# Optimization experiments

Hardware: AMD Instinct MI355X
Metric: run time of the kernel (lower is better)

Reference implementation:

```python
import jax, jax.numpy as jnp
import numpy as np

N = 60000      # total nodes
D = 300        # feature dim
R = 5          # num relations == num bases
E = 1_000_000  # edges
S = 25000      # last_idx_senses
G = 50000      # last_idx_globals
BATCH = 32


def setup_inputs() -> dict:
    key = jax.random.key(0)
    ks = jax.random.split(key, 12)
    x = jax.random.normal(ks[0], (N, D), dtype=jnp.float32)
    edge_index = jax.random.randint(ks[1], (2, E), 0, N, dtype=jnp.int32)
    edge_type = jax.random.randint(ks[2], (E,), 0, R, dtype=jnp.int32)
    current_node_index = jax.random.randint(ks[3], (BATCH,), 0, N, dtype=jnp.int32)
    scale = 1.0 / np.sqrt(D)
    # RGCNConv basis decomposition params (num_bases == num_relations)
    basis = jax.random.normal(ks[4], (R, D, D), dtype=jnp.float32) * scale
    comp = jax.random.normal(ks[5], (R, R), dtype=jnp.float32) * scale
    root = jax.random.normal(ks[6], (D, D), dtype=jnp.float32) * scale
    bias = jnp.zeros((D,), dtype=jnp.float32)
    # heads
    w_global = jax.random.normal(ks[7], (G - S, D), dtype=jnp.float32) * scale
    b_global = jnp.zeros((G - S,), dtype=jnp.float32)
    w_sense = jax.random.normal(ks[8], (S, D), dtype=jnp.float32) * scale
    b_sense = jnp.zeros((S,), dtype=jnp.float32)
    return {
        "x": x, "edge_index": edge_index, "edge_type": edge_type,
        "current_node_index": current_node_index,
        "basis": basis, "comp": comp, "root": root, "bias": bias,
        "w_global": w_global, "b_global": b_global,
        "w_sense": w_sense, "b_sense": b_sense,
    }


def reference(x, edge_index, edge_type, current_node_index,
              basis, comp, root, bias,
              w_global, b_global, w_sense, b_sense):
    src, dst = edge_index[0], edge_index[1]
    # Combined segment id over (dst node, relation): mean-aggregate source
    # features per (node, relation), then apply the per-relation transform
    # (mean(x_j) @ W_r == mean(x_j @ W_r); matches PyG RGCNConv aggr='mean').
    seg = dst * R + edge_type                      # [E]
    msg_sum = jax.ops.segment_sum(x[src], seg, num_segments=N * R)  # [N*R, D]
    cnt = jax.ops.segment_sum(jnp.ones((E,), jnp.float32), seg, num_segments=N * R)
    mean = msg_sum.reshape(N, R, D) / jnp.maximum(cnt.reshape(N, R, 1), 1.0)
    # basis decomposition: W_r = sum_b comp[r,b] * basis[b]
    W = jnp.einsum('rb,bij->rij', comp, basis)     # [R, D, D]
    agg = jnp.einsum('nrd,rde->ne', mean, W)       # [N, D]
    h = jax.nn.relu(agg + x @ root + bias)         # [N, D]
    hc = h[current_node_index]                     # [B, D]
    logits_global = hc @ w_global.T + b_global     # [B, G-S]
    logits_sense = hc @ w_sense.T + b_sense        # [B, S]
    return (jax.nn.log_softmax(logits_global, axis=-1),
            jax.nn.log_softmax(logits_sense, axis=-1))
```

## Files before the change

kernel.cpp:

```cpp
#include <hip/hip_runtime.h>
#include <hip/hip_bf16.h>
#include <math.h>

#define D 300
#define R 5
#define NE 1000000
#define B 32
#define NG 25000
#define NS 25000
#define NROWS 50000
#define NT16 3125

typedef __bf16 bf16x8 __attribute__((ext_vector_type(8)));
typedef float f32x4 __attribute__((ext_vector_type(4)));


__device__ __forceinline__ void online_upd(float& m, float& s, float v) {
    if (v > m) { s = s * __expf(m - v) + 1.0f; m = v; }
    else       { s += __expf(v - m); }
}
__device__ __forceinline__ void online_merge(float& m, float& s, float om, float os) {
    float M = fmaxf(m, om);
    s = s * __expf(m - M) + os * __expf(om - M);
    m = M;
}

__global__ void zero_ws(float4* __restrict__ p) {
    int i = blockIdx.x * 256 + threadIdx.x;
    if (i < 14441) p[i] = float4{0.f, 0.f, 0.f, 0.f};
}

__global__ __launch_bounds__(256) void scan_accum(
        const int* __restrict__ ei, const int* __restrict__ et,
        const int* __restrict__ cur, const float* __restrict__ x,
        float* __restrict__ wsum, float* __restrict__ wcnt) {
    __shared__ unsigned int tbl[32];
    __shared__ int curl[B];
    __shared__ int lcnt;
    __shared__ int2 loc[64];
    int tid = threadIdx.x;
    if (tid < 32) tbl[tid] = 0u;
    if (tid == 0) lcnt = 0;
    __syncthreads();
    if (tid < B) { int c = cur[tid]; curl[tid] = c; atomicOr(&tbl[(c >> 5) & 31], 1u << (c & 31)); }
    __syncthreads();
    long base = ((long)blockIdx.x * 256 + tid) * 4;
    if (base < NE) {
        int ds4[4];
        if (base + 4 <= NE) {
            int4 d4 = *(const int4*)(ei + NE + base);
            ds4[0] = d4.x; ds4[1] = d4.y; ds4[2] = d4.z; ds4[3] = d4.w;
        } else {
            for (int k = 0; k < 4; ++k) ds4[k] = (base + k < NE) ? ei[NE + base + k] : -1;
        }
        #pragma unroll
        for (int k = 0; k < 4; ++k) {
            int dst = ds4[k];
            if (dst < 0) continue;
            if (!(tbl[(dst >> 5) & 31] & (1u << (dst & 31)))) continue;
            int e = (int)base + k;
            int r = -1, src = 0;
            for (int b = 0; b < B; ++b) {
                if (dst == curl[b]) {
                    if (r < 0) { r = et[e]; src = ei[e]; }
                    atomicAdd(&wcnt[b * R + r], 1.0f);
                    int p = atomicAdd(&lcnt, 1);
                    if (p < 64) loc[p] = int2{src, b * R + r};
                }
            }
        }
    }
    __syncthreads();
    int n = lcnt; if (n > 64) n = 64;
    for (int m = 0; m < n; ++m) {
        int2 pr = loc[m];
        const float* xs = x + (long)pr.x * D;
        float* sm = wsum + (long)pr.y * D;
        for (int t = tid; t < D; t += 256) atomicAdd(&sm[t], xs[t]);
    }
}

__global__ __launch_bounds__(320) void rgcn_hc(
        const float* __restrict__ x, const int* __restrict__ cur,
        const float* __restrict__ comp, const float* __restrict__ root,
        const float* __restrict__ basis, const float* __restrict__ bias,
        const float* __restrict__ wsum, const float* __restrict__ wcnt,
        float* __restrict__ hcf, int* __restrict__ done, __bf16* __restrict__ hcb) {
    int kc = blockIdx.x, t = threadIdx.x;
    __shared__ float uL[800];
    __shared__ float inv[B * R];
    __shared__ float cmp[R * R];
    __shared__ int lastFlag;
    if (t < B * R) inv[t] = 1.0f / fmaxf(wcnt[t], 1.0f);
    if (t >= 160 && t < 160 + R * R) cmp[t - 160] = comp[t - 160];
    __syncthreads();
    int d0 = kc * 25;
    if (d0 < 300) {
        for (int i = t; i < 800; i += 320) {
            int b = i / 25, dd = i - b * 25;
            uL[i] = x[(long)cur[b] * D + d0 + dd];
        }
    } else {
        int g0 = d0 - 300;
        int bb = g0 / 300, t0 = g0 - bb * 300;
        for (int i = t; i < 800; i += 320) {
            int b = i / 25, dd = i - b * 25;
            float a = 0.f;
            #pragma unroll
            for (int r = 0; r < R; ++r)
                a = fmaf(cmp[r * R + bb] * inv[b * R + r], wsum[(long)(b * R + r) * D + t0 + dd], a);
            uL[i] = a;
        }
    }
    __syncthreads();
    if (t < D) {
        const float* Mb = (d0 < 300) ? (root + (long)d0 * D) : (basis + (long)(d0 - 300) * D);
        float acc[B] = {};
        #pragma unroll 5
        for (int i = 0; i < 25; ++i) {
            float m = Mb[(long)i * D + t];
            #pragma unroll
            for (int b = 0; b < B; ++b) acc[b] = fmaf(uL[b * 25 + i], m, acc[b]);
        }
        for (int b = 0; b < B; ++b) atomicAdd(&hcf[b * D + t], acc[b]);
    }
    __syncthreads();
    if (t == 0) {
        __threadfence();
        int p = atomicAdd(done, 1);
        lastFlag = (p == 71);
    }
    __syncthreads();
    if (!lastFlag) return;
    __threadfence();
    for (int i = t; i < 32 * 320; i += 320) {
        int b = i / 320, kk = i - b * 320;
        float a = 0.f;
        if (kk < D) a = fmaxf(atomicAdd(&hcf[b * D + kk], 0.0f) + bias[kk], 0.f);
        hcb[i] = (__bf16)a;
    }
}

__global__ __launch_bounds__(64) void head_gemm16(
    const __bf16* __restrict__ hcb, const float* __restrict__ wg, const float* __restrict__ bg,
    const float* __restrict__ wsn, const float* __restrict__ bsn,
    float* __restrict__ out, float2* __restrict__ pm2) {
    int l = threadIdx.x;
    int jt = blockIdx.x;
    int j0 = jt * 16;
    int ln = l & 15, og = l >> 4;

    bf16x8 bfrag0[10], bfrag1[10];
    const __bf16* hrow0 = hcb + ln * 320 + og * 8;
    const __bf16* hrow1 = hcb + (16 + ln) * 320 + og * 8;
    #pragma unroll
    for (int s = 0; s < 10; ++s) {
        bfrag0[s] = *(const bf16x8*)(hrow0 + 32 * s);
        bfrag1[s] = *(const bf16x8*)(hrow1 + 32 * s);
    }

    int row = j0 + ln;
    const float* wrow = ((row < NG) ? (wg + (long)row * D) : (wsn + (long)(row - NG) * D)) + og * 8;

    f32x4 acc0 = {}, acc1 = {};
    #pragma unroll
    for (int s = 0; s < 9; ++s) {
        float4 w0 = *(const float4*)(wrow + 32 * s);
        float4 w1 = *(const float4*)(wrow + 32 * s + 4);
        bf16x8 a;
        a[0]=(__bf16)w0.x; a[1]=(__bf16)w0.y; a[2]=(__bf16)w0.z; a[3]=(__bf16)w0.w;
        a[4]=(__bf16)w1.x; a[5]=(__bf16)w1.y; a[6]=(__bf16)w1.z; a[7]=(__bf16)w1.w;
        acc0 = __builtin_amdgcn_mfma_f32_16x16x32_bf16(a, bfrag0[s], acc0, 0, 0, 0);
        acc1 = __builtin_amdgcn_mfma_f32_16x16x32_bf16(a, bfrag1[s], acc1, 0, 0, 0);
    }
    {
        float4 w0 = float4{0.f,0.f,0.f,0.f}, w1 = float4{0.f,0.f,0.f,0.f};
        if (og == 0) { w0 = *(const float4*)(wrow + 288); w1 = *(const float4*)(wrow + 292); }
        else if (og == 1) { w0 = *(const float4*)(wrow + 288); }
        bf16x8 a;
        a[0]=(__bf16)w0.x; a[1]=(__bf16)w0.y; a[2]=(__bf16)w0.z; a[3]=(__bf16)w0.w;
        a[4]=(__bf16)w1.x; a[5]=(__bf16)w1.y; a[6]=(__bf16)w1.z; a[7]=(__bf16)w1.w;
        acc0 = __builtin_amdgcn_mfma_f32_16x16x32_bf16(a, bfrag0[9], acc0, 0, 0, 0);
        acc1 = __builtin_amdgcn_mfma_f32_16x16x32_bf16(a, bfrag1[9], acc1, 0, 0, 0);
    }

    int b0 = ln, b1 = 16 + ln;
    float m0 = -3.0e38f, s0 = 0.f, m1 = -3.0e38f, s1 = 0.f;
    float m2 = -3.0e38f, s2 = 0.f, m3 = -3.0e38f, s3 = 0.f;
    #pragma unroll
    for (int r = 0; r < 4; ++r) {
        int j = j0 + og * 4 + r;
        float bv = (j < NG) ? bg[j] : bsn[j - NG];
        float v0 = acc0[r] + bv;
        float v1 = acc1[r] + bv;
        float* op0 = (j < NG) ? (out + (long)b0 * NG + j)
                              : (out + (long)B * NG + (long)b0 * NS + (j - NG));
        float* op1 = (j < NG) ? (out + (long)b1 * NG + j)
                              : (out + (long)B * NG + (long)b1 * NS + (j - NG));
        *op0 = v0;
        *op1 = v1;
        if (j < NG) { online_upd(m0, s0, v0); online_upd(m2, s2, v1); }
        else        { online_upd(m1, s1, v0); online_upd(m3, s3, v1); }
    }
    #pragma unroll
    for (int o = 16; o <= 32; o <<= 1) {
        float t;
        t = __shfl_xor(m0, o); { float ts = __shfl_xor(s0, o); online_merge(m0, s0, t, ts); }
        t = __shfl_xor(m1, o); { float ts = __shfl_xor(s1, o); online_merge(m1, s1, t, ts); }
        t = __shfl_xor(m2, o); { float ts = __shfl_xor(s2, o); online_merge(m2, s2, t, ts); }
        t = __shfl_xor(m3, o); { float ts = __shfl_xor(s3, o); online_merge(m3, s3, t, ts); }
    }
    if (og == 0) {
        pm2[(long)b0 * NT16 + jt]       = float2{m0, s0};
        pm2[(long)(B + b0) * NT16 + jt] = float2{m1, s1};
        pm2[(long)b1 * NT16 + jt]       = float2{m2, s2};
        pm2[(long)(B + b1) * NT16 + jt] = float2{m3, s3};
    }
}

__global__ __launch_bounds__(256) void lse_red(const float2* __restrict__ pm2,
                                               float* __restrict__ lse) {
    int rw = blockIdx.x, tid = threadIdx.x;
    const float2* pr = pm2 + (long)rw * NT16;
    float m = -3.0e38f, s = 0.f;
    for (int i = tid; i < NT16; i += 256) { float2 e = pr[i]; online_merge(m, s, e.x, e.y); }
    #pragma unroll
    for (int o = 32; o; o >>= 1) {
        float om = __shfl_xor(m, o), os = __shfl_xor(s, o);
        online_merge(m, s, om, os);
    }
    __shared__ float sm[4], ss[4];
    if ((tid & 63) == 0) { sm[tid >> 6] = m; ss[tid >> 6] = s; }
    __syncthreads();
    if (tid == 0) {
        float M = sm[0], S = ss[0];
        for (int w = 1; w < 4; ++w) online_merge(M, S, sm[w], ss[w]);
        lse[rw] = M + __logf(S);
    }
}

__global__ __launch_bounds__(256) void sub_lse(float* __restrict__ out,
                                               const float* __restrict__ lse) {
    int rw = blockIdx.x / 25, c = blockIdx.x % 25;
    float l = lse[rw];
    float4* o4 = (float4*)out + (long)rw * 6250 + c * 250;
    int tid = threadIdx.x;
    if (tid < 250) { float4 v = o4[tid]; v.x -= l; v.y -= l; v.z -= l; v.w -= l; o4[tid] = v; }
}

extern "C" void kernel_launch(void* const* d_in, const int* in_sizes, int n_in,
                              void* d_out, int out_size, void* d_ws, size_t ws_size,
                              hipStream_t stream) {
    const float* x     = (const float*)d_in[0];
    const int*   ei    = (const int*)d_in[1];
    const int*   et    = (const int*)d_in[2];
    const int*   cur   = (const int*)d_in[3];
    const float* basis = (const float*)d_in[4];
    const float* comp  = (const float*)d_in[5];
    const float* root  = (const float*)d_in[6];
    const float* bias  = (const float*)d_in[7];
    const float* wg    = (const float*)d_in[8];
    const float* bgl   = (const float*)d_in[9];
    const float* wsn   = (const float*)d_in[10];
    const float* bsn   = (const float*)d_in[11];
    float* out  = (float*)d_out;
    float* wsf  = (float*)d_ws;
    float*  wsum = wsf;
    float*  wcnt = wsf + 48000;
    float*  hcf  = wsf + 48160;
    int*    done = (int*)(wsf + 57760);
    __bf16* hcb  = (__bf16*)(wsf + 57764);
    float2* pm2  = (float2*)(wsf + 62884);
    float*  lse  = wsf + 462884;

    zero_ws<<<57, 256, 0, stream>>>((float4*)d_ws);
    scan_accum<<<977, 256, 0, stream>>>(ei, et, cur, x, wsum, wcnt);
    rgcn_hc<<<72, 320, 0, stream>>>(x, cur, comp, root, basis, bias, wsum, wcnt, hcf, done, hcb);
    head_gemm16<<<NT16, 64, 0, stream>>>(hcb, wg, bgl, wsn, bsn, out, pm2);
    lse_red<<<64, 256, 0, stream>>>(pm2, lse);
    sub_lse<<<1600, 256, 0, stream>>>(out, lse);
}
```

Measured before the change: 80.29 us.

## Restructure pipeline: drop zero kernel, match-list scan, fuse finalize and LSE stages

The global zeroing kernel is removed; the edge scan now only records matching (src, slot) pairs per block into a compact list and zeroes hcf itself. Each rgcn_hc basis block gathers that list and accumulates neighbour sums and counts in shared memory, so the global atomics and the last-block finalize with its threadfence are gone. The ReLU/bias/bf16 conversion of hc moves into head_gemm, which now runs four waves per block and stages hc in padded LDS. The LSE reduction is merged with the subtraction. Together this cuts the launch count from six to four. The trade-off is that every basis block redundantly scans the match list and re-gathers x rows, and the per-block cap of 16 matches (1024 in total) could drop edges on heavier inputs.

```diff
diff --git a/kernel.cpp b/kernel.cpp
--- a/kernel.cpp
+++ b/kernel.cpp
@@ -10,6 +10,9 @@
 #define NS 25000
 #define NROWS 50000
 #define NT16 3125
+#define NSB 977
+#define MCAP 16
+#define HST 324
 
 typedef __bf16 bf16x8 __attribute__((ext_vector_type(8)));
 typedef float f32x4 __attribute__((ext_vector_type(4)));
@@ -25,20 +28,17 @@
     m = M;
 }
 
-__global__ void zero_ws(float4* __restrict__ p) {
-    int i = blockIdx.x * 256 + threadIdx.x;
-    if (i < 14441) p[i] = float4{0.f, 0.f, 0.f, 0.f};
-}
-
-__global__ __launch_bounds__(256) void scan_accum(
+__global__ __launch_bounds__(256) void scan_match(
         const int* __restrict__ ei, const int* __restrict__ et,
-        const int* __restrict__ cur, const float* __restrict__ x,
-        float* __restrict__ wsum, float* __restrict__ wcnt) {
+        const int* __restrict__ cur,
+        int2* __restrict__ mlist, int* __restrict__ mcntb, float* __restrict__ hcf) {
     __shared__ unsigned int tbl[32];
     __shared__ int curl[B];
     __shared__ int lcnt;
-    __shared__ int2 loc[64];
+    __shared__ int2 loc[MCAP];
     int tid = threadIdx.x;
+    int gidx = blockIdx.x * 256 + tid;
+    if (gidx < 9600) hcf[gidx] = 0.f;
     if (tid < 32) tbl[tid] = 0u;
     if (tid == 0) lcnt = 0;
     __syncthreads();
@@ -63,58 +63,81 @@
             for (int b = 0; b < B; ++b) {
                 if (dst == curl[b]) {
                     if (r < 0) { r = et[e]; src = ei[e]; }
-                    atomicAdd(&wcnt[b * R + r], 1.0f);
                     int p = atomicAdd(&lcnt, 1);
-                    if (p < 64) loc[p] = int2{src, b * R + r};
+                    if (p < MCAP) loc[p] = int2{src, b * R + r};
                 }
             }
         }
     }
     __syncthreads();
-    int n = lcnt; if (n > 64) n = 64;
-    for (int m = 0; m < n; ++m) {
-        int2 pr = loc[m];
-        const float* xs = x + (long)pr.x * D;
-        float* sm = wsum + (long)pr.y * D;
-        for (int t = tid; t < D; t += 256) atomicAdd(&sm[t], xs[t]);
-    }
+    int n = lcnt < MCAP ? lcnt : MCAP;
+    if (tid == 0) mcntb[blockIdx.x] = n;
+    if (tid < n) mlist[blockIdx.x * MCAP + tid] = loc[tid];
 }
 
 __global__ __launch_bounds__(320) void rgcn_hc(
         const float* __restrict__ x, const int* __restrict__ cur,
         const float* __restrict__ comp, const float* __restrict__ root,
-        const float* __restrict__ basis, const float* __restrict__ bias,
-        const float* __restrict__ wsum, const float* __restrict__ wcnt,
-        float* __restrict__ hcf, int* __restrict__ done, __bf16* __restrict__ hcb) {
+        const float* __restrict__ basis,
+        const int2* __restrict__ mlist, const int* __restrict__ mcntb,
+        float* __restrict__ hcf) {
     int kc = blockIdx.x, t = threadIdx.x;
     __shared__ float uL[800];
-    __shared__ float inv[B * R];
+    __shared__ int2 ml[1024];
+    __shared__ int mn;
+    __shared__ float wsumL[160 * 25];
+    __shared__ float cntL[160];
+    __shared__ float invL[160];
     __shared__ float cmp[R * R];
-    __shared__ int lastFlag;
-    if (t < B * R) inv[t] = 1.0f / fmaxf(wcnt[t], 1.0f);
-    if (t >= 160 && t < 160 + R * R) cmp[t - 160] = comp[t - 160];
-    __syncthreads();
     int d0 = kc * 25;
-    if (d0 < 300) {
+
+    if (kc < 12) {
         for (int i = t; i < 800; i += 320) {
             int b = i / 25, dd = i - b * 25;
             uL[i] = x[(long)cur[b] * D + d0 + dd];
         }
+        __syncthreads();
     } else {
-        int g0 = d0 - 300;
-        int bb = g0 / 300, t0 = g0 - bb * 300;
+        if (t == 0) mn = 0;
+        if (t < R * R) cmp[t] = comp[t];
+        for (int i = t; i < 160; i += 320) cntL[i] = 0.f;
+        for (int i = t; i < 160 * 25; i += 320) wsumL[i] = 0.f;
+        __syncthreads();
+        for (int i = t; i < NSB; i += 320) {
+            int c = mcntb[i];
+            for (int k = 0; k < c; ++k) {
+                int p = atomicAdd(&mn, 1);
+                if (p < 1024) ml[p] = mlist[i * MCAP + k];
+            }
+        }
+        __syncthreads();
+        int n = mn < 1024 ? mn : 1024;
+        for (int m = t; m < n; m += 320) atomicAdd(&cntL[ml[m].y], 1.0f);
+        __syncthreads();
+        for (int i = t; i < 160; i += 320) invL[i] = 1.0f / fmaxf(cntL[i], 1.0f);
+        int g2 = kc - 12;
+        int bb = g2 / 12, t0 = (g2 - bb * 12) * 25;
+        if (t < 300) {
+            int g = t / 25, col = t - g * 25;
+            for (int m = g; m < n; m += 12) {
+                int2 pr = ml[m];
+                atomicAdd(&wsumL[pr.y * 25 + col], x[(long)pr.x * D + t0 + col]);
+            }
+        }
+        __syncthreads();
         for (int i = t; i < 800; i += 320) {
             int b = i / 25, dd = i - b * 25;
             float a = 0.f;
             #pragma unroll
             for (int r = 0; r < R; ++r)
-                a = fmaf(cmp[r * R + bb] * inv[b * R + r], wsum[(long)(b * R + r) * D + t0 + dd], a);
+                a = fmaf(cmp[r * R + bb] * invL[b * R + r], wsumL[(b * R + r) * 25 + dd], a);
             uL[i] = a;
         }
-    }
-    __syncthreads();
+        __syncthreads();
+    }
+
     if (t < D) {
-        const float* Mb = (d0 < 300) ? (root + (long)d0 * D) : (basis + (long)(d0 - 300) * D);
+        const float* Mb = (kc < 12) ? (root + (long)d0 * D) : (basis + (long)(d0 - 300) * D);
         float acc[B] = {};
         #pragma unroll 5
         for (int i = 0; i < 25; ++i) {
@@ -124,35 +147,31 @@
         }
         for (int b = 0; b < B; ++b) atomicAdd(&hcf[b * D + t], acc[b]);
     }
-    __syncthreads();
-    if (t == 0) {
-        __threadfence();
-        int p = atomicAdd(done, 1);
-        lastFlag = (p == 71);
-    }
-    __syncthreads();
-    if (!lastFlag) return;
-    __threadfence();
-    for (int i = t; i < 32 * 320; i += 320) {
-        int b = i / 320, kk = i - b * 320;
-        float a = 0.f;
-        if (kk < D) a = fmaxf(atomicAdd(&hcf[b * D + kk], 0.0f) + bias[kk], 0.f);
-        hcb[i] = (__bf16)a;
-    }
-}
-
-__global__ __launch_bounds__(64) void head_gemm16(
-    const __bf16* __restrict__ hcb, const float* __restrict__ wg, const float* __restrict__ bg,
+}
+
+__global__ __launch_bounds__(256) void head_gemm(
+    const float* __restrict__ hcf, const float* __restrict__ bias,
+    const float* __restrict__ wg, const float* __restrict__ bg,
     const float* __restrict__ wsn, const float* __restrict__ bsn,
     float* __restrict__ out, float2* __restrict__ pm2) {
-    int l = threadIdx.x;
-    int jt = blockIdx.x;
+    __shared__ __bf16 hcbL[32 * HST];
+    int tid = threadIdx.x;
+    for (int i = tid; i < 32 * HST; i += 256) {
+        int b = i / HST, kk = i - b * HST;
+        float v = 0.f;
+        if (kk < D) v = fmaxf(hcf[b * D + kk] + bias[kk], 0.f);
+        hcbL[i] = (__bf16)v;
+    }
+    __syncthreads();
+
+    int wid = tid >> 6, l = tid & 63, ln = l & 15, og = l >> 4;
+    int jt = blockIdx.x * 4 + wid;
+    if (jt >= NT16) return;
     int j0 = jt * 16;
-    int ln = l & 15, og = l >> 4;
 
     bf16x8 bfrag0[10], bfrag1[10];
-    const __bf16* hrow0 = hcb + ln * 320 + og * 8;
-    const __bf16* hrow1 = hcb + (16 + ln) * 320 + og * 8;
+    const __bf16* hrow0 = hcbL + ln * HST + og * 8;
+    const __bf16* hrow1 = hcbL + (16 + ln) * HST + og * 8;
     #pragma unroll
     for (int s = 0; s < 10; ++s) {
         bfrag0[s] = *(const bf16x8*)(hrow0 + 32 * s);
@@ -204,11 +223,11 @@
     }
     #pragma unroll
     for (int o = 16; o <= 32; o <<= 1) {
-        float t;
-        t = __shfl_xor(m0, o); { float ts = __shfl_xor(s0, o); online_merge(m0, s0, t, ts); }
-        t = __shfl_xor(m1, o); { float ts = __shfl_xor(s1, o); online_merge(m1, s1, t, ts); }
-        t = __shfl_xor(m2, o); { float ts = __shfl_xor(s2, o); online_merge(m2, s2, t, ts); }
-        t = __shfl_xor(m3, o); { float ts = __shfl_xor(s3, o); online_merge(m3, s3, t, ts); }
+        float tm, ts;
+        tm = __shfl_xor(m0, o); ts = __shfl_xor(s0, o); online_merge(m0, s0, tm, ts);
+        tm = __shfl_xor(m1, o); ts = __shfl_xor(s1, o); online_merge(m1, s1, tm, ts);
+        tm = __shfl_xor(m2, o); ts = __shfl_xor(s2, o); online_merge(m2, s2, tm, ts);
+        tm = __shfl_xor(m3, o); ts = __shfl_xor(s3, o); online_merge(m3, s3, tm, ts);
     }
     if (og == 0) {
         pm2[(long)b0 * NT16 + jt]       = float2{m0, s0};
@@ -218,9 +237,10 @@
     }
 }
 
-__global__ __launch_bounds__(256) void lse_red(const float2* __restrict__ pm2,
-                                               float* __restrict__ lse) {
-    int rw = blockIdx.x, tid = threadIdx.x;
+__global__ __launch_bounds__(256) void lse_sub(float* __restrict__ out,
+                                               const float2* __restrict__ pm2) {
+    int rw = blockIdx.x / 25, c = blockIdx.x % 25;
+    int tid = threadIdx.x;
     const float2* pr = pm2 + (long)rw * NT16;
     float m = -3.0e38f, s = 0.f;
     for (int i = tid; i < NT16; i += 256) { float2 e = pr[i]; online_merge(m, s, e.x, e.y); }
@@ -230,21 +250,17 @@
         online_merge(m, s, om, os);
     }
     __shared__ float sm[4], ss[4];
+    __shared__ float lseS;
     if ((tid & 63) == 0) { sm[tid >> 6] = m; ss[tid >> 6] = s; }
     __syncthreads();
     if (tid == 0) {
         float M = sm[0], S = ss[0];
         for (int w = 1; w < 4; ++w) online_merge(M, S, sm[w], ss[w]);
-        lse[rw] = M + __logf(S);
-    }
-}
-
-__global__ __launch_bounds__(256) void sub_lse(float* __restrict__ out,
-                                               const float* __restrict__ lse) {
-    int rw = blockIdx.x / 25, c = blockIdx.x % 25;
-    float l = lse[rw];
+        lseS = M + __logf(S);
+    }
+    __syncthreads();
+    float l = lseS;
     float4* o4 = (float4*)out + (long)rw * 6250 + c * 250;
-    int tid = threadIdx.x;
     if (tid < 250) { float4 v = o4[tid]; v.x -= l; v.y -= l; v.z -= l; v.w -= l; o4[tid] = v; }
 }
 
@@ -265,18 +281,13 @@
     const float* bsn   = (const float*)d_in[11];
     float* out  = (float*)d_out;
     float* wsf  = (float*)d_ws;
-    float*  wsum = wsf;
-    float*  wcnt = wsf + 48000;
-    float*  hcf  = wsf + 48160;
-    int*    done = (int*)(wsf + 57760);
-    __bf16* hcb  = (__bf16*)(wsf + 57764);
-    float2* pm2  = (float2*)(wsf + 62884);
-    float*  lse  = wsf + 462884;
-
-    zero_ws<<<57, 256, 0, stream>>>((float4*)d_ws);
-    scan_accum<<<977, 256, 0, stream>>>(ei, et, cur, x, wsum, wcnt);
-    rgcn_hc<<<72, 320, 0, stream>>>(x, cur, comp, root, basis, bias, wsum, wcnt, hcf, done, hcb);
-    head_gemm16<<<NT16, 64, 0, stream>>>(hcb, wg, bgl, wsn, bsn, out, pm2);
-    lse_red<<<64, 256, 0, stream>>>(pm2, lse);
-    sub_lse<<<1600, 256, 0, stream>>>(out, lse);
-}
+    float*  hcf   = wsf;
+    float2* pm2   = (float2*)(wsf + 9600);
+    int*    mcntb = (int*)(wsf + 409600);
+    int2*   mlist = (int2*)(wsf + 410578);
+
+    scan_match<<<NSB, 256, 0, stream>>>(ei, et, cur, mlist, mcntb, hcf);
+    rgcn_hc<<<72, 320, 0, stream>>>(x, cur, comp, root, basis, mlist, mcntb, hcf);
+    head_gemm<<<(NT16 + 3) / 4, 256, 0, stream>>>(hcf, bias, wg, bgl, wsn, bsn, out, pm2);
+    lse_sub<<<1600, 256, 0, stream>>>(out, pm2);
+}
```

Measured after the change: 91.75 us. +14.3%, slower.

## Fuse bias/ReLU into head GEMM via LDS, merge LSE reduce with subtract

Applied to the files above, without the earlier changes.

Removes the last-block completion counter in rgcn_hc. Bias, ReLU and the bf16 conversion of hc now happen inside the head GEMM, which stages hc in padded LDS and runs four waves per block, each issuing all of its weight-row loads up front behind a sched_barrier. The separate LSE reduction kernel is merged into the subtract kernel, so each of the 1600 blocks recomputes its row's LSE from the partials. This cuts one launch and the serialized tail, at the cost of redundant LSE reductions and per-block hc staging.

```diff
diff --git a/kernel.cpp b/kernel.cpp
--- a/kernel.cpp
+++ b/kernel.cpp
@@ -10,6 +10,7 @@
 #define NS 25000
 #define NROWS 50000
 #define NT16 3125
+#define HST 324
 
 typedef __bf16 bf16x8 __attribute__((ext_vector_type(8)));
 typedef float f32x4 __attribute__((ext_vector_type(4)));
@@ -27,7 +28,7 @@
 
 __global__ void zero_ws(float4* __restrict__ p) {
     int i = blockIdx.x * 256 + threadIdx.x;
-    if (i < 14441) p[i] = float4{0.f, 0.f, 0.f, 0.f};
+    if (i < 14440) p[i] = float4{0.f, 0.f, 0.f, 0.f};
 }
 
 __global__ __launch_bounds__(256) void scan_accum(
@@ -83,14 +84,12 @@
 __global__ __launch_bounds__(320) void rgcn_hc(
         const float* __restrict__ x, const int* __restrict__ cur,
         const float* __restrict__ comp, const float* __restrict__ root,
-        const float* __restrict__ basis, const float* __restrict__ bias,
-        const float* __restrict__ wsum, const float* __restrict__ wcnt,
-        float* __restrict__ hcf, int* __restrict__ done, __bf16* __restrict__ hcb) {
+        const float* __restrict__ basis, const float* __restrict__ wsum,
+        const float* __restrict__ wcnt, float* __restrict__ hcf) {
     int kc = blockIdx.x, t = threadIdx.x;
     __shared__ float uL[800];
     __shared__ float inv[B * R];
     __shared__ float cmp[R * R];
-    __shared__ int lastFlag;
     if (t < B * R) inv[t] = 1.0f / fmaxf(wcnt[t], 1.0f);
     if (t >= 160 && t < 160 + R * R) cmp[t - 160] = comp[t - 160];
     __syncthreads();
@@ -124,64 +123,55 @@
         }
         for (int b = 0; b < B; ++b) atomicAdd(&hcf[b * D + t], acc[b]);
     }
-    __syncthreads();
-    if (t == 0) {
-        __threadfence();
-        int p = atomicAdd(done, 1);
-        lastFlag = (p == 71);
-    }
-    __syncthreads();
-    if (!lastFlag) return;
-    __threadfence();
-    for (int i = t; i < 32 * 320; i += 320) {
-        int b = i / 320, kk = i - b * 320;
-        float a = 0.f;
-        if (kk < D) a = fmaxf(atomicAdd(&hcf[b * D + kk], 0.0f) + bias[kk], 0.f);
-        hcb[i] = (__bf16)a;
-    }
-}
-
-__global__ __launch_bounds__(64) void head_gemm16(
-    const __bf16* __restrict__ hcb, const float* __restrict__ wg, const float* __restrict__ bg,
+}
+
+__global__ __launch_bounds__(256) void head_gemm(
+    const float* __restrict__ hcf, const float* __restrict__ bias,
+    const float* __restrict__ wg, const float* __restrict__ bg,
     const float* __restrict__ wsn, const float* __restrict__ bsn,
     float* __restrict__ out, float2* __restrict__ pm2) {
-    int l = threadIdx.x;
-    int jt = blockIdx.x;
+    __shared__ __bf16 hcbL[32 * HST];
+    int tid = threadIdx.x;
+    for (int i = tid; i < 32 * HST; i += 256) {
+        int b = i / HST, kk = i - b * HST;
+        float v = 0.f;
+        if (kk < D) v = fmaxf(hcf[b * D + kk] + bias[kk], 0.f);
+        hcbL[i] = (__bf16)v;
+    }
+    __syncthreads();
+
+    int wid = tid >> 6, l = tid & 63, ln = l & 15, og = l >> 4;
+    int jt = blockIdx.x * 4 + wid;
+    if (jt >= NT16) return;
     int j0 = jt * 16;
-    int ln = l & 15, og = l >> 4;
-
-    bf16x8 bfrag0[10], bfrag1[10];
-    const __bf16* hrow0 = hcb + ln * 320 + og * 8;
-    const __bf16* hrow1 = hcb + (16 + ln) * 320 + og * 8;
-    #pragma unroll
-    for (int s = 0; s < 10; ++s) {
-        bfrag0[s] = *(const bf16x8*)(hrow0 + 32 * s);
-        bfrag1[s] = *(const bf16x8*)(hrow1 + 32 * s);
-    }
-
     int row = j0 + ln;
     const float* wrow = ((row < NG) ? (wg + (long)row * D) : (wsn + (long)(row - NG) * D)) + og * 8;
 
+    float4 w[20];
+    #pragma unroll
+    for (int s = 0; s < 9; ++s) {
+        w[2 * s]     = *(const float4*)(wrow + 32 * s);
+        w[2 * s + 1] = *(const float4*)(wrow + 32 * s + 4);
+    }
+    {
+        w[18] = float4{0.f, 0.f, 0.f, 0.f};
+        w[19] = float4{0.f, 0.f, 0.f, 0.f};
+        if (og == 0) { w[18] = *(const float4*)(wrow + 288); w[19] = *(const float4*)(wrow + 292); }
+        else if (og == 1) { w[18] = *(const float4*)(wrow + 288); }
+    }
+    __builtin_amdgcn_sched_barrier(0);
+
+    const __bf16* hrow0 = hcbL + ln * HST + og * 8;
+    const __bf16* hrow1 = hcbL + (16 + ln) * HST + og * 8;
     f32x4 acc0 = {}, acc1 = {};
     #pragma unroll
-    for (int s = 0; s < 9; ++s) {
-        float4 w0 = *(const float4*)(wrow + 32 * s);
-        float4 w1 = *(const float4*)(wrow + 32 * s + 4);
+    for (int s = 0; s < 10; ++s) {
+        float4 w0 = w[2 * s], w1 = w[2 * s + 1];
         bf16x8 a;
         a[0]=(__bf16)w0.x; a[1]=(__bf16)w0.y; a[2]=(__bf16)w0.z; a[3]=(__bf16)w0.w;
         a[4]=(__bf16)w1.x; a[5]=(__bf16)w1.y; a[6]=(__bf16)w1.z; a[7]=(__bf16)w1.w;
-        acc0 = __builtin_amdgcn_mfma_f32_16x16x32_bf16(a, bfrag0[s], acc0, 0, 0, 0);
-        acc1 = __builtin_amdgcn_mfma_f32_16x16x32_bf16(a, bfrag1[s], acc1, 0, 0, 0);
-    }
-    {
-        float4 w0 = float4{0.f,0.f,0.f,0.f}, w1 = float4{0.f,0.f,0.f,0.f};
-        if (og == 0) { w0 = *(const float4*)(wrow + 288); w1 = *(const float4*)(wrow + 292); }
-        else if (og == 1) { w0 = *(const float4*)(wrow + 288); }
-        bf16x8 a;
-        a[0]=(__bf16)w0.x; a[1]=(__bf16)w0.y; a[2]=(__bf16)w0.z; a[3]=(__bf16)w0.w;
-        a[4]=(__bf16)w1.x; a[5]=(__bf16)w1.y; a[6]=(__bf16)w1.z; a[7]=(__bf16)w1.w;
-        acc0 = __builtin_amdgcn_mfma_f32_16x16x32_bf16(a, bfrag0[9], acc0, 0, 0, 0);
-        acc1 = __builtin_amdgcn_mfma_f32_16x16x32_bf16(a, bfrag1[9], acc1, 0, 0, 0);
+        acc0 = __builtin_amdgcn_mfma_f32_16x16x32_bf16(a, *(const bf16x8*)(hrow0 + 32 * s), acc0, 0, 0, 0);
+        acc1 = __builtin_amdgcn_mfma_f32_16x16x32_bf16(a, *(const bf16x8*)(hrow1 + 32 * s), acc1, 0, 0, 0);
     }
 
     int b0 = ln, b1 = 16 + ln;
@@ -204,11 +194,11 @@
     }
     #pragma unroll
     for (int o = 16; o <= 32; o <<= 1) {
-        float t;
-        t = __shfl_xor(m0, o); { float ts = __shfl_xor(s0, o); online_merge(m0, s0, t, ts); }
-        t = __shfl_xor(m1, o); { float ts = __shfl_xor(s1, o); online_merge(m1, s1, t, ts); }
-        t = __shfl_xor(m2, o); { float ts = __shfl_xor(s2, o); online_merge(m2, s2, t, ts); }
-        t = __shfl_xor(m3, o); { float ts = __shfl_xor(s3, o); online_merge(m3, s3, t, ts); }
+        float tm, ts;
+        tm = __shfl_xor(m0, o); ts = __shfl_xor(s0, o); online_merge(m0, s0, tm, ts);
+        tm = __shfl_xor(m1, o); ts = __shfl_xor(s1, o); online_merge(m1, s1, tm, ts);
+        tm = __shfl_xor(m2, o); ts = __shfl_xor(s2, o); online_merge(m2, s2, tm, ts);
+        tm = __shfl_xor(m3, o); ts = __shfl_xor(s3, o); online_merge(m3, s3, tm, ts);
     }
     if (og == 0) {
         pm2[(long)b0 * NT16 + jt]       = float2{m0, s0};
@@ -218,9 +208,10 @@
     }
 }
 
-__global__ __launch_bounds__(256) void lse_red(const float2* __restrict__ pm2,
-                                               float* __restrict__ lse) {
-    int rw = blockIdx.x, tid = threadIdx.x;
+__global__ __launch_bounds__(256) void lse_sub(float* __restrict__ out,
+                                               const float2* __restrict__ pm2) {
+    int rw = blockIdx.x / 25, c = blockIdx.x % 25;
+    int tid = threadIdx.x;
     const float2* pr = pm2 + (long)rw * NT16;
     float m = -3.0e38f, s = 0.f;
     for (int i = tid; i < NT16; i += 256) { float2 e = pr[i]; online_merge(m, s, e.x, e.y); }
@@ -230,21 +221,17 @@
         online_merge(m, s, om, os);
     }
     __shared__ float sm[4], ss[4];
+    __shared__ float lseS;
     if ((tid & 63) == 0) { sm[tid >> 6] = m; ss[tid >> 6] = s; }
     __syncthreads();
     if (tid == 0) {
         float M = sm[0], S = ss[0];
         for (int w = 1; w < 4; ++w) online_merge(M, S, sm[w], ss[w]);
-        lse[rw] = M + __logf(S);
-    }
-}
-
-__global__ __launch_bounds__(256) void sub_lse(float* __restrict__ out,
-                                               const float* __restrict__ lse) {
-    int rw = blockIdx.x / 25, c = blockIdx.x % 25;
-    float l = lse[rw];
+        lseS = M + __logf(S);
+    }
+    __syncthreads();
+    float l = lseS;
     float4* o4 = (float4*)out + (long)rw * 6250 + c * 250;
-    int tid = threadIdx.x;
     if (tid < 250) { float4 v = o4[tid]; v.x -= l; v.y -= l; v.z -= l; v.w -= l; o4[tid] = v; }
 }
 
@@ -268,15 +255,11 @@
     float*  wsum = wsf;
     float*  wcnt = wsf + 48000;
     float*  hcf  = wsf + 48160;
-    int*    done = (int*)(wsf + 57760);
-    __bf16* hcb  = (__bf16*)(wsf + 57764);
-    float2* pm2  = (float2*)(wsf + 62884);
-    float*  lse  = wsf + 462884;
+    float2* pm2  = (float2*)(wsf + 57760);
 
     zero_ws<<<57, 256, 0, stream>>>((float4*)d_ws);
     scan_accum<<<977, 256, 0, stream>>>(ei, et, cur, x, wsum, wcnt);
-    rgcn_hc<<<72, 320, 0, stream>>>(x, cur, comp, root, basis, bias, wsum, wcnt, hcf, done, hcb);
-    head_gemm16<<<NT16, 64, 0, stream>>>(hcb, wg, bgl, wsn, bsn, out, pm2);
-    lse_red<<<64, 256, 0, stream>>>(pm2, lse);
-    sub_lse<<<1600, 256, 0, stream>>>(out, lse);
-}
+    rgcn_hc<<<72, 320, 0, stream>>>(x, cur, comp, root, basis, wsum, wcnt, hcf);
+    head_gemm<<<(NT16 + 3) / 4, 256, 0, stream>>>(hcf, bias, wg, bgl, wsn, bsn, out, pm2);
+    lse_sub<<<1600, 256, 0, stream>>>(out, pm2);
+}
```

Result: faster. 74.70 us (-7.0%).
